# Kernel tuning notes

Hardware: AMD Instinct MI355X
Metric: run time of the kernel (lower is better)

Reference implementation:

```python
import jax, jax.numpy as jnp
import numpy as np

N = 100000
D = 128
E = 1600000
NUM_STEPS = 8
LAM0 = 1.0
LAM1 = 1.0
ALPHA = 1.0 / (1.0 + 0.0 + LAM0 + LAM1)  # args.alp == 0 path


def setup_inputs() -> dict:
    key = jax.random.key(0)
    ks = jax.random.split(key, 12)
    X = jax.random.normal(ks[0], (N, D), dtype=jnp.float32)
    # H init: normal(0, 1/in_features) + I  (notresidual=False branch)
    H1 = jax.random.normal(ks[1], (D, D), dtype=jnp.float32) * (1.0 / D) + jnp.eye(D, dtype=jnp.float32)
    H2 = jax.random.normal(ks[2], (D, D), dtype=jnp.float32) * (1.0 / D) + jnp.eye(D, dtype=jnp.float32)
    w_beta = jax.random.uniform(ks[3], (E,), dtype=jnp.float32)
    w_gamma = jax.random.uniform(ks[4], (E,), dtype=jnp.float32)
    d_beta = jax.random.uniform(ks[5], (N,), dtype=jnp.float32)
    d_gamma = jax.random.uniform(ks[6], (N,), dtype=jnp.float32)
    src_beta = jax.random.randint(ks[7], (E,), 0, N, dtype=jnp.int32)
    dst_beta = jax.random.randint(ks[8], (E,), 0, N, dtype=jnp.int32)
    src_gamma = jax.random.randint(ks[9], (E,), 0, N, dtype=jnp.int32)
    dst_gamma = jax.random.randint(ks[10], (E,), 0, N, dtype=jnp.int32)
    return {"X": X, "H1": H1, "H2": H2, "w_beta": w_beta, "w_gamma": w_gamma,
            "d_beta": d_beta, "d_gamma": d_gamma,
            "src_beta": src_beta, "dst_beta": dst_beta,
            "src_gamma": src_gamma, "dst_gamma": dst_gamma}


def _spmm(w, src, dst, Y):
    # (sparse A) @ Y with A[dst, src] = w
    return jax.ops.segment_sum(w[:, None] * Y[src], dst, num_segments=N)


def reference(X, H1, H2, w_beta, w_gamma, d_beta, d_gamma,
              src_beta, dst_beta, src_gamma, dst_gamma):
    # Q_tild = lam0*D_beta + lam1*D_gamma + I  (diagonal)
    q = LAM0 * d_beta + LAM1 * d_gamma + 1.0  # [N]
    S1 = H1 + H1.T
    P1 = H1 @ H1.T
    S2 = H2 + H2.T
    P2 = H2 @ H2.T
    Y0 = X
    Y = X
    for _ in range(NUM_STEPS):
        AbY = _spmm(w_beta, src_beta, dst_beta, Y)    # A_beta @ Y
        AgY = _spmm(w_gamma, src_gamma, dst_gamma, Y)  # A_gamma @ Y
        term_beta = AbY @ S1 - d_beta[:, None] * (Y @ P1)
        # L_gamma @ Y = D_gamma@Y - A_gamma@Y
        term_gamma = (d_gamma[:, None] * Y - AgY
                      + AgY @ S2 - d_gamma[:, None] * (Y @ P2))
        Y_hat = LAM0 * term_beta + Y0 + LAM1 * term_gamma
        Y = (1.0 - ALPHA) * Y + ALPHA * (Y_hat / q[:, None])
    return Y
```

## Files before the change

### kernel.cpp

```cpp
#include <hip/hip_runtime.h>
#include <cstdint>
#include <cstddef>

#define DD 128
#define ATS 68
#define BQS 132


__global__ void count2_k(const int* __restrict__ dstb, const int* __restrict__ dstg,
                         int* __restrict__ degb, int* __restrict__ degg, int E, int gE) {
    int b = blockIdx.x;
    const int* dst = (b < gE) ? dstb : dstg;
    int* deg = (b < gE) ? degb : degg;
    int i = ((b < gE) ? b : b - gE) * blockDim.x + threadIdx.x;
    if (i < E) atomicAdd(&deg[dst[i]], 1);
}

__global__ __launch_bounds__(1024) void scan2_k(const int* __restrict__ degb,
                                                const int* __restrict__ degg,
                                                int* __restrict__ rpb, int* __restrict__ rpg,
                                                int* __restrict__ curb, int* __restrict__ curg,
                                                int n) {
    const int* deg = (blockIdx.x == 0) ? degb : degg;
    int* rp = (blockIdx.x == 0) ? rpb : rpg;
    int* cur = (blockIdx.x == 0) ? curb : curg;
    __shared__ int sums[1024];
    int tid = threadIdx.x;
    int per = (n + 1023) >> 10;
    int start = tid * per;
    int end = min(start + per, n);
    int s = 0;
    for (int i = start; i < end; ++i) s += deg[i];
    sums[tid] = s;
    __syncthreads();
    for (int off = 1; off < 1024; off <<= 1) {
        int v = (tid >= off) ? sums[tid - off] : 0;
        __syncthreads();
        sums[tid] += v;
        __syncthreads();
    }
    int pre = (tid == 0) ? 0 : sums[tid - 1];
    for (int i = start; i < end; ++i) {
        rp[i] = pre;
        cur[i] = pre;
        pre += deg[i];
    }
    if (end == n) rp[n] = pre;
}

__global__ void fill2_k(const int* __restrict__ srcb, const int* __restrict__ dstb,
                        const float* __restrict__ wb,
                        const int* __restrict__ srcg, const int* __restrict__ dstg,
                        const float* __restrict__ wg,
                        int* __restrict__ curb, int* __restrict__ curg,
                        int2* __restrict__ eb, int2* __restrict__ eg, int E, int gE) {
    int b = blockIdx.x;
    bool isb = (b < gE);
    const int* src = isb ? srcb : srcg;
    const int* dst = isb ? dstb : dstg;
    const float* w = isb ? wb : wg;
    int* cur = isb ? curb : curg;
    int2* edges = isb ? eb : eg;
    int i = (isb ? b : b - gE) * blockDim.x + threadIdx.x;
    if (i < E) {
        int d = dst[i];
        int pos = atomicAdd(&cur[d], 1);
        edges[pos] = make_int2(src[i], __float_as_int(w[i]));
    }
}


__global__ __launch_bounds__(256) void prep_k(const float* __restrict__ H,
                                              float* __restrict__ P,
                                              float* __restrict__ S) {
    int idx = blockIdx.x * 256 + threadIdx.x;
    int i = idx >> 7, j = idx & 127;
    float acc = 0.f;
    for (int k = 0; k < DD; ++k) acc += H[i * DD + k] * H[j * DD + k];
    P[idx] = acc;
    S[idx] = H[i * DD + j] + H[j * DD + i];
}


__global__ __launch_bounds__(256, 8) void spmm2_k(
    const int* __restrict__ rpb, const int2* __restrict__ eb,
    const int* __restrict__ rpg, const int2* __restrict__ eg,
    const float* __restrict__ Y,
    float* __restrict__ outb, float* __restrict__ outg, int n)
{
    int node = blockIdx.x * 4 + (threadIdx.x >> 6);
    if (node >= n) return;
    int lane = threadIdx.x & 63;

    int jb = rpb[node], be = rpb[node + 1];
    int jg = rpg[node], ge = rpg[node + 1];
    float b0 = 0.f, b1 = 0.f, g0 = 0.f, g1 = 0.f;

    while (jb + 4 <= be && jg + 4 <= ge) {
        int2 x0 = eb[jb + 0], x1 = eb[jb + 1], x2 = eb[jb + 2], x3 = eb[jb + 3];
        int2 y0 = eg[jg + 0], y1 = eg[jg + 1], y2 = eg[jg + 2], y3 = eg[jg + 3];
        float2 fb0 = *((const float2*)(Y + (size_t)x0.x * DD) + lane);
        float2 fb1 = *((const float2*)(Y + (size_t)x1.x * DD) + lane);
        float2 fb2 = *((const float2*)(Y + (size_t)x2.x * DD) + lane);
        float2 fb3 = *((const float2*)(Y + (size_t)x3.x * DD) + lane);
        float2 fg0 = *((const float2*)(Y + (size_t)y0.x * DD) + lane);
        float2 fg1 = *((const float2*)(Y + (size_t)y1.x * DD) + lane);
        float2 fg2 = *((const float2*)(Y + (size_t)y2.x * DD) + lane);
        float2 fg3 = *((const float2*)(Y + (size_t)y3.x * DD) + lane);
        float wb0 = __int_as_float(x0.y), wb1 = __int_as_float(x1.y);
        float wb2 = __int_as_float(x2.y), wb3 = __int_as_float(x3.y);
        float wg0 = __int_as_float(y0.y), wg1 = __int_as_float(y1.y);
        float wg2 = __int_as_float(y2.y), wg3 = __int_as_float(y3.y);
        b0 += wb0 * fb0.x; b1 += wb0 * fb0.y;
        b0 += wb1 * fb1.x; b1 += wb1 * fb1.y;
        b0 += wb2 * fb2.x; b1 += wb2 * fb2.y;
        b0 += wb3 * fb3.x; b1 += wb3 * fb3.y;
        g0 += wg0 * fg0.x; g1 += wg0 * fg0.y;
        g0 += wg1 * fg1.x; g1 += wg1 * fg1.y;
        g0 += wg2 * fg2.x; g1 += wg2 * fg2.y;
        g0 += wg3 * fg3.x; g1 += wg3 * fg3.y;
        jb += 4; jg += 4;
    }
    while (jb + 4 <= be) {
        int2 x0 = eb[jb + 0], x1 = eb[jb + 1], x2 = eb[jb + 2], x3 = eb[jb + 3];
        float2 f0 = *((const float2*)(Y + (size_t)x0.x * DD) + lane);
        float2 f1 = *((const float2*)(Y + (size_t)x1.x * DD) + lane);
        float2 f2 = *((const float2*)(Y + (size_t)x2.x * DD) + lane);
        float2 f3 = *((const float2*)(Y + (size_t)x3.x * DD) + lane);
        float w0 = __int_as_float(x0.y), w1 = __int_as_float(x1.y);
        float w2 = __int_as_float(x2.y), w3 = __int_as_float(x3.y);
        b0 += w0 * f0.x; b1 += w0 * f0.y;
        b0 += w1 * f1.x; b1 += w1 * f1.y;
        b0 += w2 * f2.x; b1 += w2 * f2.y;
        b0 += w3 * f3.x; b1 += w3 * f3.y;
        jb += 4;
    }
    while (jg + 4 <= ge) {
        int2 y0 = eg[jg + 0], y1 = eg[jg + 1], y2 = eg[jg + 2], y3 = eg[jg + 3];
        float2 f0 = *((const float2*)(Y + (size_t)y0.x * DD) + lane);
        float2 f1 = *((const float2*)(Y + (size_t)y1.x * DD) + lane);
        float2 f2 = *((const float2*)(Y + (size_t)y2.x * DD) + lane);
        float2 f3 = *((const float2*)(Y + (size_t)y3.x * DD) + lane);
        float w0 = __int_as_float(y0.y), w1 = __int_as_float(y1.y);
        float w2 = __int_as_float(y2.y), w3 = __int_as_float(y3.y);
        g0 += w0 * f0.x; g1 += w0 * f0.y;
        g0 += w1 * f1.x; g1 += w1 * f1.y;
        g0 += w2 * f2.x; g1 += w2 * f2.y;
        g0 += w3 * f3.x; g1 += w3 * f3.y;
        jg += 4;
    }
    for (; jb < be; ++jb) {
        int2 e = eb[jb];
        float2 f = *((const float2*)(Y + (size_t)e.x * DD) + lane);
        float wv = __int_as_float(e.y);
        b0 += wv * f.x; b1 += wv * f.y;
    }
    for (; jg < ge; ++jg) {
        int2 e = eg[jg];
        float2 f = *((const float2*)(Y + (size_t)e.x * DD) + lane);
        float wv = __int_as_float(e.y);
        g0 += wv * f.x; g1 += wv * f.y;
    }
    *((float2*)(outb + (size_t)node * DD) + lane) = make_float2(b0, b1);
    *((float2*)(outg + (size_t)node * DD) + lane) = make_float2(g0, g1);
}


__global__ __launch_bounds__(256, 3) void dense4_k(
    const float* __restrict__ Yc, const float* __restrict__ X,
    const float* __restrict__ AbY, const float* __restrict__ AgY,
    const float* __restrict__ db, const float* __restrict__ dg,
    const float* __restrict__ P1, const float* __restrict__ P2,
    const float* __restrict__ S1, const float* __restrict__ S2,
    float* __restrict__ Yn, int n)
{
    __shared__ float At[DD * ATS];
    __shared__ float U[32 * BQS];

    const int tid = threadIdx.x;
    const int cg = tid & 15;
    const int rg = tid >> 4;
    const int row0 = blockIdx.x * 64;

    float aS[4][8], aP1[4][8], aP2[4][8];
#pragma unroll
    for (int i = 0; i < 4; ++i)
#pragma unroll
        for (int j = 0; j < 8; ++j) { aS[i][j] = 0.f; aP1[i][j] = 0.f; aP2[i][j] = 0.f; }

    auto stageT = [&](const float* __restrict__ G) {
        int r = tid >> 2;
        int rowc = min(row0 + r, n - 1);
        const float* gp = G + (size_t)rowc * DD;
#pragma unroll
        for (int i = 0; i < 8; ++i) {
            int c = ((tid & 3) << 2) + (i << 4);
            float4 v = *reinterpret_cast<const float4*>(gp + c);
            At[(c + 0) * ATS + r] = v.x;
            At[(c + 1) * ATS + r] = v.y;
            At[(c + 2) * ATS + r] = v.z;
            At[(c + 3) * ATS + r] = v.w;
        }
    };
    auto gemm = [&](const float* __restrict__ M, float (&acc)[4][8]) {
#pragma unroll 1
        for (int kq = 0; kq < 4; ++kq) {
            {
                int kl = tid & 31;
                int cb = (tid >> 5) * 16;
                const float* gp = M + (size_t)(kq * 32 + kl) * DD + cb;
                float* bp = U + kl * BQS + cb;
#pragma unroll
                for (int u = 0; u < 4; ++u)
                    *reinterpret_cast<float4*>(bp + 4 * u) =
                        *reinterpret_cast<const float4*>(gp + 4 * u);
            }
            __syncthreads();
#pragma unroll 2
            for (int kl = 0; kl < 32; ++kl) {
                int k = kq * 32 + kl;
                float4 a = *reinterpret_cast<const float4*>(&At[k * ATS + rg * 4]);
                float4 b0 = *reinterpret_cast<const float4*>(&U[kl * BQS + cg * 4]);
                float4 b1 = *reinterpret_cast<const float4*>(&U[kl * BQS + 64 + cg * 4]);
                float av[4] = {a.x, a.y, a.z, a.w};
                float bv[8] = {b0.x, b0.y, b0.z, b0.w, b1.x, b1.y, b1.z, b1.w};
#pragma unroll
                for (int i = 0; i < 4; ++i)
#pragma unroll
                    for (int j = 0; j < 8; ++j) acc[i][j] += av[i] * bv[j];
            }
            __syncthreads();
        }
    };

    stageT(AbY);
    __syncthreads();
    gemm(S1, aS);

    stageT(AgY);
    __syncthreads();
    gemm(S2, aS);
#pragma unroll
    for (int i = 0; i < 4; ++i) {
        int r = rg * 4 + i;
#pragma unroll
        for (int j = 0; j < 8; ++j) {
            int c = (j >> 2) * 64 + cg * 4 + (j & 3);
            aS[i][j] -= At[c * ATS + r];
        }
    }
    __syncthreads();

    stageT(Yc);
    __syncthreads();
    gemm(P1, aP1);
    gemm(P2, aP2);

    const float AL = 1.0f / 3.0f;
#pragma unroll
    for (int i = 0; i < 4; ++i) {
        int row = row0 + rg * 4 + i;
        if (row < n) {
            float dbv = db[row], dgv = dg[row];
            float aq = AL / (dbv + dgv + 1.0f);
#pragma unroll
            for (int hh = 0; hh < 2; ++hh) {
                size_t off = (size_t)row * DD + hh * 64 + cg * 4;
                float4 y = *reinterpret_cast<const float4*>(Yc + off);
                float4 x = *reinterpret_cast<const float4*>(X + off);
                float yv[4] = {y.x, y.y, y.z, y.w};
                float xv[4] = {x.x, x.y, x.z, x.w};
                float ov[4];
#pragma unroll
                for (int q = 0; q < 4; ++q) {
                    int j = hh * 4 + q;
                    float yhat = aS[i][j] + xv[q] + dgv * yv[q]
                                 - dbv * aP1[i][j] - dgv * aP2[i][j];
                    ov[q] = (1.0f - AL) * yv[q] + yhat * aq;
                }
                *reinterpret_cast<float4*>(Yn + off) = make_float4(ov[0], ov[1], ov[2], ov[3]);
            }
        }
    }
}


extern "C" void kernel_launch(void* const* d_in, const int* in_sizes, int n_in,
                              void* d_out, int out_size, void* d_ws, size_t ws_size,
                              hipStream_t stream) {
    const float* X   = (const float*)d_in[0];
    const float* H1  = (const float*)d_in[1];
    const float* H2  = (const float*)d_in[2];
    const float* wb  = (const float*)d_in[3];
    const float* wg  = (const float*)d_in[4];
    const float* db  = (const float*)d_in[5];
    const float* dg  = (const float*)d_in[6];
    const int* srcb  = (const int*)d_in[7];
    const int* dstb  = (const int*)d_in[8];
    const int* srcg  = (const int*)d_in[9];
    const int* dstg  = (const int*)d_in[10];
    const int N = in_sizes[5];
    const int E = in_sizes[3];
    float* Yout = (float*)d_out;

    char* p = (char*)d_ws;
    auto alloc = [&](size_t b) -> void* {
        void* r = (void*)p;
        p += (b + 255) & ~(size_t)255;
        return r;
    };
    float* P1 = (float*)alloc((size_t)DD * DD * 4);
    float* S1 = (float*)alloc((size_t)DD * DD * 4);
    float* P2 = (float*)alloc((size_t)DD * DD * 4);
    float* S2 = (float*)alloc((size_t)DD * DD * 4);
    int* degb = (int*)alloc((size_t)N * 4);
    int* degg = (int*)alloc((size_t)N * 4);
    int* rpb  = (int*)alloc((size_t)(N + 1) * 4);
    int* rpg  = (int*)alloc((size_t)(N + 1) * 4);
    int* curb = (int*)alloc((size_t)N * 4);
    int* curg = (int*)alloc((size_t)N * 4);
    int2* eb  = (int2*)alloc((size_t)E * 8);
    int2* eg  = (int2*)alloc((size_t)E * 8);
    float* AbY = (float*)alloc((size_t)N * DD * 4);
    float* AgY = (float*)alloc((size_t)N * DD * 4);
    float* Yw  = (float*)alloc((size_t)N * DD * 4);

    hipMemsetAsync(degb, 0, (size_t)N * 4, stream);
    hipMemsetAsync(degg, 0, (size_t)N * 4, stream);

    int gE = (E + 255) / 256;
    count2_k<<<2 * gE, 256, 0, stream>>>(dstb, dstg, degb, degg, E, gE);
    scan2_k<<<2, 1024, 0, stream>>>(degb, degg, rpb, rpg, curb, curg, N);
    fill2_k<<<2 * gE, 256, 0, stream>>>(srcb, dstb, wb, srcg, dstg, wg,
                                        curb, curg, eb, eg, E, gE);
    prep_k<<<64, 256, 0, stream>>>(H1, P1, S1);
    prep_k<<<64, 256, 0, stream>>>(H2, P2, S2);

    const float* Ycur = X;
    float* Ybufs[2] = {Yw, Yout};
    int gs = (N + 3) / 4;
    int gd = (N + 63) / 64;
    for (int s = 0; s < 8; ++s) {
        float* Yn = Ybufs[s & 1];
        spmm2_k<<<gs, 256, 0, stream>>>(rpb, eb, rpg, eg, Ycur, AbY, AgY, N);
        dense4_k<<<gd, 256, 0, stream>>>(Ycur, X, AbY, AgY, db, dg,
                                         P1, P2, S1, S2, Yn, N);
        Ycur = Yn;
    }
}
```

Before: 3.955 ms.

## Reorder dense kernel: fused P1/P2 GEMM first, fold into accumulator, prefetch B tiles

The dense update kernel now runs the Y@P1 and Y@P2 GEMMs first in one fused loop over k that shares the A-tile read, then folds them with X, d_gamma*Y and the diagonal terms into a single accumulator. That same accumulator then takes the AbY@S1 and AgY@S2 products, so one 32-float accumulator array is dropped. This lowers register pressure, which matters under launch_bounds(256,3). Both GEMM loops also prefetch the next B tile from global memory into registers while computing on the current one, to hide load latency. In exchange, the fused P loop stages two B tiles per phase and adds more barriers.

```diff
diff --git a/kernel.cpp b/kernel.cpp
--- a/kernel.cpp
+++ b/kernel.cpp
@@ -182,12 +182,6 @@
     const int rg = tid >> 4;
     const int row0 = blockIdx.x * 64;
 
-    float aS[4][8], aP1[4][8], aP2[4][8];
-#pragma unroll
-    for (int i = 0; i < 4; ++i)
-#pragma unroll
-        for (int j = 0; j < 8; ++j) { aS[i][j] = 0.f; aP1[i][j] = 0.f; aP2[i][j] = 0.f; }
-
     auto stageT = [&](const float* __restrict__ G) {
         int r = tid >> 2;
         int rowc = min(row0 + r, n - 1);
@@ -202,26 +196,124 @@
             At[(c + 3) * ATS + r] = v.w;
         }
     };
-    auto gemm = [&](const float* __restrict__ M, float (&acc)[4][8]) {
+
+    float aP1[4][8], aP2[4][8];
+#pragma unroll
+    for (int i = 0; i < 4; ++i)
+#pragma unroll
+        for (int j = 0; j < 8; ++j) { aP1[i][j] = 0.f; aP2[i][j] = 0.f; }
+
+    stageT(Yc);
+
+    {
+        const int kl = tid >> 4;
+        const int cb = (tid & 15) * 8;
+        float4 p1a, p1b, p2a, p2b;
+        {
+            const float* g1 = P1 + (size_t)kl * DD + cb;
+            const float* g2 = P2 + (size_t)kl * DD + cb;
+            p1a = *reinterpret_cast<const float4*>(g1);
+            p1b = *reinterpret_cast<const float4*>(g1 + 4);
+            p2a = *reinterpret_cast<const float4*>(g2);
+            p2b = *reinterpret_cast<const float4*>(g2 + 4);
+        }
+#pragma unroll 1
+        for (int ph = 0; ph < 8; ++ph) {
+            __syncthreads();
+            {
+                float* b1 = U + kl * BQS + cb;
+                float* b2 = U + (16 + kl) * BQS + cb;
+                *reinterpret_cast<float4*>(b1) = p1a;
+                *reinterpret_cast<float4*>(b1 + 4) = p1b;
+                *reinterpret_cast<float4*>(b2) = p2a;
+                *reinterpret_cast<float4*>(b2 + 4) = p2b;
+            }
+            __syncthreads();
+            if (ph < 7) {
+                const float* g1 = P1 + (size_t)((ph + 1) * 16 + kl) * DD + cb;
+                const float* g2 = P2 + (size_t)((ph + 1) * 16 + kl) * DD + cb;
+                p1a = *reinterpret_cast<const float4*>(g1);
+                p1b = *reinterpret_cast<const float4*>(g1 + 4);
+                p2a = *reinterpret_cast<const float4*>(g2);
+                p2b = *reinterpret_cast<const float4*>(g2 + 4);
+            }
+#pragma unroll 2
+            for (int k2 = 0; k2 < 16; ++k2) {
+                int k = ph * 16 + k2;
+                float4 a = *reinterpret_cast<const float4*>(&At[k * ATS + rg * 4]);
+                float4 b10 = *reinterpret_cast<const float4*>(&U[k2 * BQS + cg * 4]);
+                float4 b11 = *reinterpret_cast<const float4*>(&U[k2 * BQS + 64 + cg * 4]);
+                float4 b20 = *reinterpret_cast<const float4*>(&U[(16 + k2) * BQS + cg * 4]);
+                float4 b21 = *reinterpret_cast<const float4*>(&U[(16 + k2) * BQS + 64 + cg * 4]);
+                float av[4] = {a.x, a.y, a.z, a.w};
+                float b1v[8] = {b10.x, b10.y, b10.z, b10.w, b11.x, b11.y, b11.z, b11.w};
+                float b2v[8] = {b20.x, b20.y, b20.z, b20.w, b21.x, b21.y, b21.z, b21.w};
+#pragma unroll
+                for (int i = 0; i < 4; ++i)
+#pragma unroll
+                    for (int j = 0; j < 8; ++j) {
+                        aP1[i][j] += av[i] * b1v[j];
+                        aP2[i][j] += av[i] * b2v[j];
+                    }
+            }
+        }
+        __syncthreads();
+    }
+
+#pragma unroll
+    for (int i = 0; i < 4; ++i) {
+        int rowc = min(row0 + rg * 4 + i, n - 1);
+        float dbv = db[rowc], dgv = dg[rowc];
+#pragma unroll
+        for (int hh = 0; hh < 2; ++hh) {
+            size_t off = (size_t)rowc * DD + hh * 64 + cg * 4;
+            float4 y = *reinterpret_cast<const float4*>(Yc + off);
+            float4 x = *reinterpret_cast<const float4*>(X + off);
+            float yv[4] = {y.x, y.y, y.z, y.w};
+            float xv[4] = {x.x, x.y, x.z, x.w};
+#pragma unroll
+            for (int q = 0; q < 4; ++q) {
+                int j = hh * 4 + q;
+                aP1[i][j] = xv[q] + dgv * yv[q] - dbv * aP1[i][j] - dgv * aP2[i][j];
+            }
+        }
+    }
+
+    auto gemm1 = [&](const float* __restrict__ M, float (&acc)[4][8]) {
+        const int kl = tid & 31;
+        const int cb = (tid >> 5) * 16;
+        float4 pa, pb, pc, pd;
+        {
+            const float* gp = M + (size_t)kl * DD + cb;
+            pa = *reinterpret_cast<const float4*>(gp);
+            pb = *reinterpret_cast<const float4*>(gp + 4);
+            pc = *reinterpret_cast<const float4*>(gp + 8);
+            pd = *reinterpret_cast<const float4*>(gp + 12);
+        }
 #pragma unroll 1
         for (int kq = 0; kq < 4; ++kq) {
+            __syncthreads();
             {
-                int kl = tid & 31;
-                int cb = (tid >> 5) * 16;
-                const float* gp = M + (size_t)(kq * 32 + kl) * DD + cb;
                 float* bp = U + kl * BQS + cb;
-#pragma unroll
-                for (int u = 0; u < 4; ++u)
-                    *reinterpret_cast<float4*>(bp + 4 * u) =
-                        *reinterpret_cast<const float4*>(gp + 4 * u);
+                *reinterpret_cast<float4*>(bp) = pa;
+                *reinterpret_cast<float4*>(bp + 4) = pb;
+                *reinterpret_cast<float4*>(bp + 8) = pc;
+                *reinterpret_cast<float4*>(bp + 12) = pd;
             }
             __syncthreads();
+            if (kq < 3) {
+                const float* gp = M + (size_t)((kq + 1) * 32 + kl) * DD + cb;
+                pa = *reinterpret_cast<const float4*>(gp);
+                pb = *reinterpret_cast<const float4*>(gp + 4);
+                pc = *reinterpret_cast<const float4*>(gp + 8);
+                pd = *reinterpret_cast<const float4*>(gp + 12);
+            }
 #pragma unroll 2
-            for (int kl = 0; kl < 32; ++kl) {
-                int k = kq * 32 + kl;
+            for (int k2 = 0; k2 < 32; ++k2) {
+                int k = kq * 32 + k2;
                 float4 a = *reinterpret_cast<const float4*>(&At[k * ATS + rg * 4]);
-                float4 b0 = *reinterpret_cast<const float4*>(&U[kl * BQS + cg * 4]);
-                float4 b1 = *reinterpret_cast<const float4*>(&U[kl * BQS + 64 + cg * 4]);
+                float4 b0 = *reinterpret_cast<const float4*>(&U[k2 * BQS + cg * 4]);
+                float4 b1 = *reinterpret_cast<const float4*>(&U[k2 * BQS + 64 + cg * 4]);
                 float av[4] = {a.x, a.y, a.z, a.w};
                 float bv[8] = {b0.x, b0.y, b0.z, b0.w, b1.x, b1.y, b1.z, b1.w};
 #pragma unroll
@@ -229,32 +321,24 @@
 #pragma unroll
                     for (int j = 0; j < 8; ++j) acc[i][j] += av[i] * bv[j];
             }
-            __syncthreads();
-        }
+        }
+        __syncthreads();
     };
 
     stageT(AbY);
-    __syncthreads();
-    gemm(S1, aS);
+    gemm1(S1, aP1);
 
     stageT(AgY);
-    __syncthreads();
-    gemm(S2, aS);
+    gemm1(S2, aP1);
 #pragma unroll
     for (int i = 0; i < 4; ++i) {
         int r = rg * 4 + i;
 #pragma unroll
         for (int j = 0; j < 8; ++j) {
             int c = (j >> 2) * 64 + cg * 4 + (j & 3);
-            aS[i][j] -= At[c * ATS + r];
-        }
-    }
-    __syncthreads();
-
-    stageT(Yc);
-    __syncthreads();
-    gemm(P1, aP1);
-    gemm(P2, aP2);
+            aP1[i][j] -= At[c * ATS + r];
+        }
+    }
 
     const float AL = 1.0f / 3.0f;
 #pragma unroll
@@ -267,16 +351,12 @@
             for (int hh = 0; hh < 2; ++hh) {
                 size_t off = (size_t)row * DD + hh * 64 + cg * 4;
                 float4 y = *reinterpret_cast<const float4*>(Yc + off);
-                float4 x = *reinterpret_cast<const float4*>(X + off);
                 float yv[4] = {y.x, y.y, y.z, y.w};
-                float xv[4] = {x.x, x.y, x.z, x.w};
                 float ov[4];
 #pragma unroll
                 for (int q = 0; q < 4; ++q) {
                     int j = hh * 4 + q;
-                    float yhat = aS[i][j] + xv[q] + dgv * yv[q]
-                                 - dbv * aP1[i][j] - dgv * aP2[i][j];
-                    ov[q] = (1.0f - AL) * yv[q] + yhat * aq;
+                    ov[q] = (1.0f - AL) * yv[q] + aP1[i][j] * aq;
                 }
                 *reinterpret_cast<float4*>(Yn + off) = make_float4(ov[0], ov[1], ov[2], ov[3]);
             }
```

Result: no change. 3.916 ms (-1.0%).

## Restructure dense step with wave-uniform weight columns read via scalar loads

Applied to the files above, without the earlier changes.

The dense kernel now runs 1024-thread blocks, one row per lane and 8 output columns per wave. Weight matrix entries are wave-uniform (readfirstlane on the column offset), so they can be fetched with scalar loads instead of being staged through a shared-memory tile, and the P1/P2 products are fused into one pass over the Y tile. Output is transposed through LDS for coalesced stores. The trade-off is a much smaller per-thread register tile (8 accumulators instead of 96), which lowers FMA reuse per LDS read, plus dependence on scalar-cache bandwidth for the weights.

```diff
diff --git a/kernel.cpp b/kernel.cpp
--- a/kernel.cpp
+++ b/kernel.cpp
@@ -4,7 +4,7 @@
 
 #define DD 128
 #define ATS 68
-#define BQS 132
+#define WTS 130
 
 
 __global__ void count2_k(const int* __restrict__ dstb, const int* __restrict__ dstg,
@@ -166,7 +166,7 @@
 }
 
 
-__global__ __launch_bounds__(256, 3) void dense4_k(
+__global__ __launch_bounds__(1024, 8) void dense_vs_k(
     const float* __restrict__ Yc, const float* __restrict__ X,
     const float* __restrict__ AbY, const float* __restrict__ AgY,
     const float* __restrict__ db, const float* __restrict__ dg,
@@ -175,111 +175,121 @@
     float* __restrict__ Yn, int n)
 {
     __shared__ float At[DD * ATS];
-    __shared__ float U[32 * BQS];
-
-    const int tid = threadIdx.x;
-    const int cg = tid & 15;
-    const int rg = tid >> 4;
+
+    const int tid  = threadIdx.x;
+    const int lane = tid & 63;
+    const int wid  = tid >> 6;
+    const int cw   = wid << 3;
+    const int c0   = __builtin_amdgcn_readfirstlane(cw);
     const int row0 = blockIdx.x * 64;
-
-    float aS[4][8], aP1[4][8], aP2[4][8];
-#pragma unroll
-    for (int i = 0; i < 4; ++i)
-#pragma unroll
-        for (int j = 0; j < 8; ++j) { aS[i][j] = 0.f; aP1[i][j] = 0.f; aP2[i][j] = 0.f; }
+    const int rowc = min(row0 + lane, n - 1);
 
     auto stageT = [&](const float* __restrict__ G) {
-        int r = tid >> 2;
-        int rowc = min(row0 + r, n - 1);
-        const float* gp = G + (size_t)rowc * DD;
-#pragma unroll
-        for (int i = 0; i < 8; ++i) {
-            int c = ((tid & 3) << 2) + (i << 4);
-            float4 v = *reinterpret_cast<const float4*>(gp + c);
-            At[(c + 0) * ATS + r] = v.x;
-            At[(c + 1) * ATS + r] = v.y;
-            At[(c + 2) * ATS + r] = v.z;
-            At[(c + 3) * ATS + r] = v.w;
+        const float* gp = G + (size_t)rowc * DD + cw;
+        float4 v0 = *reinterpret_cast<const float4*>(gp);
+        float4 v1 = *reinterpret_cast<const float4*>(gp + 4);
+        At[(cw + 0) * ATS + lane] = v0.x;
+        At[(cw + 1) * ATS + lane] = v0.y;
+        At[(cw + 2) * ATS + lane] = v0.z;
+        At[(cw + 3) * ATS + lane] = v0.w;
+        At[(cw + 4) * ATS + lane] = v1.x;
+        At[(cw + 5) * ATS + lane] = v1.y;
+        At[(cw + 6) * ATS + lane] = v1.z;
+        At[(cw + 7) * ATS + lane] = v1.w;
+    };
+
+    const float dbv = db[rowc];
+    const float dgv = dg[rowc];
+
+    float acc[8];
+
+    stageT(Yc);
+    __syncthreads();
+
+    {
+        const float* xp = X + (size_t)rowc * DD + c0;
+#pragma unroll
+        for (int j = 0; j < 8; ++j)
+            acc[j] = xp[j] + dgv * At[(c0 + j) * ATS + lane];
+    }
+
+    {
+        const float* p1 = P1 + c0;
+        const float* p2 = P2 + c0;
+#pragma unroll 4
+        for (int k = 0; k < DD; ++k) {
+            float a = At[k * ATS + lane];
+            float am1 = dbv * a;
+            float am2 = dgv * a;
+            const float* r1 = p1 + k * DD;
+            const float* r2 = p2 + k * DD;
+#pragma unroll
+            for (int j = 0; j < 8; ++j)
+                acc[j] -= am1 * r1[j] + am2 * r2[j];
         }
-    };
-    auto gemm = [&](const float* __restrict__ M, float (&acc)[4][8]) {
-#pragma unroll 1
-        for (int kq = 0; kq < 4; ++kq) {
-            {
-                int kl = tid & 31;
-                int cb = (tid >> 5) * 16;
-                const float* gp = M + (size_t)(kq * 32 + kl) * DD + cb;
-                float* bp = U + kl * BQS + cb;
-#pragma unroll
-                for (int u = 0; u < 4; ++u)
-                    *reinterpret_cast<float4*>(bp + 4 * u) =
-                        *reinterpret_cast<const float4*>(gp + 4 * u);
-            }
-            __syncthreads();
-#pragma unroll 2
-            for (int kl = 0; kl < 32; ++kl) {
-                int k = kq * 32 + kl;
-                float4 a = *reinterpret_cast<const float4*>(&At[k * ATS + rg * 4]);
-                float4 b0 = *reinterpret_cast<const float4*>(&U[kl * BQS + cg * 4]);
-                float4 b1 = *reinterpret_cast<const float4*>(&U[kl * BQS + 64 + cg * 4]);
-                float av[4] = {a.x, a.y, a.z, a.w};
-                float bv[8] = {b0.x, b0.y, b0.z, b0.w, b1.x, b1.y, b1.z, b1.w};
-#pragma unroll
-                for (int i = 0; i < 4; ++i)
-#pragma unroll
-                    for (int j = 0; j < 8; ++j) acc[i][j] += av[i] * bv[j];
-            }
-            __syncthreads();
+    }
+
+    __syncthreads();
+    stageT(AbY);
+    __syncthreads();
+    {
+        const float* s1 = S1 + c0;
+#pragma unroll 4
+        for (int k = 0; k < DD; ++k) {
+            float a = At[k * ATS + lane];
+            const float* r = s1 + k * DD;
+#pragma unroll
+            for (int j = 0; j < 8; ++j)
+                acc[j] += a * r[j];
         }
-    };
-
-    stageT(AbY);
-    __syncthreads();
-    gemm(S1, aS);
-
+    }
+
+    __syncthreads();
     stageT(AgY);
     __syncthreads();
-    gemm(S2, aS);
-#pragma unroll
-    for (int i = 0; i < 4; ++i) {
-        int r = rg * 4 + i;
-#pragma unroll
-        for (int j = 0; j < 8; ++j) {
-            int c = (j >> 2) * 64 + cg * 4 + (j & 3);
-            aS[i][j] -= At[c * ATS + r];
+    {
+        const float* s2 = S2 + c0;
+#pragma unroll 4
+        for (int k = 0; k < DD; ++k) {
+            float a = At[k * ATS + lane];
+            const float* r = s2 + k * DD;
+#pragma unroll
+            for (int j = 0; j < 8; ++j)
+                acc[j] += a * r[j];
         }
-    }
-    __syncthreads();
-
-    stageT(Yc);
-    __syncthreads();
-    gemm(P1, aP1);
-    gemm(P2, aP2);
-
-    const float AL = 1.0f / 3.0f;
-#pragma unroll
-    for (int i = 0; i < 4; ++i) {
-        int row = row0 + rg * 4 + i;
-        if (row < n) {
-            float dbv = db[row], dgv = dg[row];
-            float aq = AL / (dbv + dgv + 1.0f);
-#pragma unroll
-            for (int hh = 0; hh < 2; ++hh) {
-                size_t off = (size_t)row * DD + hh * 64 + cg * 4;
-                float4 y = *reinterpret_cast<const float4*>(Yc + off);
-                float4 x = *reinterpret_cast<const float4*>(X + off);
-                float yv[4] = {y.x, y.y, y.z, y.w};
-                float xv[4] = {x.x, x.y, x.z, x.w};
-                float ov[4];
-#pragma unroll
-                for (int q = 0; q < 4; ++q) {
-                    int j = hh * 4 + q;
-                    float yhat = aS[i][j] + xv[q] + dgv * yv[q]
-                                 - dbv * aP1[i][j] - dgv * aP2[i][j];
-                    ov[q] = (1.0f - AL) * yv[q] + yhat * aq;
-                }
-                *reinterpret_cast<float4*>(Yn + off) = make_float4(ov[0], ov[1], ov[2], ov[3]);
-            }
+#pragma unroll
+        for (int j = 0; j < 8; ++j)
+            acc[j] -= At[(c0 + j) * ATS + lane];
+    }
+
+    {
+        const float aq = (1.0f / 3.0f) / (dbv + dgv + 1.0f);
+        const float* yp = Yc + (size_t)rowc * DD + c0;
+#pragma unroll
+        for (int j = 0; j < 8; ++j)
+            acc[j] = (2.0f / 3.0f) * yp[j] + acc[j] * aq;
+    }
+
+    __syncthreads();
+    {
+        float* W = At;
+#pragma unroll
+        for (int j = 0; j < 8; ++j)
+            W[lane * WTS + cw + j] = acc[j];
+    }
+    __syncthreads();
+    {
+        const float* W = At;
+        int r2 = tid >> 4;
+        int c2 = (tid & 15) << 3;
+        int row2 = row0 + r2;
+        if (row2 < n) {
+            float ov[8];
+#pragma unroll
+            for (int j = 0; j < 8; ++j) ov[j] = W[r2 * WTS + c2 + j];
+            float* op = Yn + (size_t)row2 * DD + c2;
+            *reinterpret_cast<float4*>(op) = make_float4(ov[0], ov[1], ov[2], ov[3]);
+            *reinterpret_cast<float4*>(op + 4) = make_float4(ov[4], ov[5], ov[6], ov[7]);
         }
     }
 }
@@ -343,8 +353,8 @@
     for (int s = 0; s < 8; ++s) {
         float* Yn = Ybufs[s & 1];
         spmm2_k<<<gs, 256, 0, stream>>>(rpb, eb, rpg, eg, Ycur, AbY, AgY, N);
-        dense4_k<<<gd, 256, 0, stream>>>(Ycur, X, AbY, AgY, db, dg,
-                                         P1, P2, S1, S2, Yn, N);
+        dense_vs_k<<<gd, 1024, 0, stream>>>(Ycur, X, AbY, AgY, db, dg,
+                                            P1, P2, S1, S2, Yn, N);
         Ycur = Yn;
     }
 }
```

New measurement: 4.438 ms. 12.2% more time.

## Fuse dense stage into one K=512 GEMM over concatenated operand matrix

Applied to the files above, without the earlier changes.

Concatenates S1, S2-I, -P1, -P2 into a single 512x128 B matrix and streams [AbY | AgY | db*Y | dg*Y] as a K=512 A operand, so one accumulator replaces three and the -AgY term folds into S2. Shared memory for the A tile shrinks to a 32-row slab, and launch bounds rise to 6 blocks per CU to raise occupancy. The reciprocal q factor is precomputed once into a buffer. The cost is more loop iterations, each with its own sync, and per-element scaling while staging the tile.

```diff
diff --git a/kernel.cpp b/kernel.cpp
--- a/kernel.cpp
+++ b/kernel.cpp
@@ -3,8 +3,8 @@
 #include <cstddef>
 
 #define DD 128
-#define ATS 68
-#define BQS 132
+#define ATS2 68
+#define BQS2 132
 
 
 __global__ void count2_k(const int* __restrict__ dstb, const int* __restrict__ dstg,
@@ -71,14 +71,23 @@
 
 
 __global__ __launch_bounds__(256) void prep_k(const float* __restrict__ H,
-                                              float* __restrict__ P,
-                                              float* __restrict__ S) {
+                                              float* __restrict__ Pdst,
+                                              float* __restrict__ Sdst,
+                                              int sub_ident) {
     int idx = blockIdx.x * 256 + threadIdx.x;
     int i = idx >> 7, j = idx & 127;
     float acc = 0.f;
     for (int k = 0; k < DD; ++k) acc += H[i * DD + k] * H[j * DD + k];
-    P[idx] = acc;
-    S[idx] = H[i * DD + j] + H[j * DD + i];
+    Pdst[idx] = -acc;
+    float s = H[i * DD + j] + H[j * DD + i];
+    if (sub_ident && i == j) s -= 1.0f;
+    Sdst[idx] = s;
+}
+
+__global__ void aq_k(const float* __restrict__ db, const float* __restrict__ dg,
+                     float* __restrict__ aq, int n) {
+    int i = blockIdx.x * blockDim.x + threadIdx.x;
+    if (i < n) aq[i] = (1.0f / 3.0f) / (db[i] + dg[i] + 1.0f);
 }
 
 
@@ -166,103 +175,86 @@
 }
 
 
-__global__ __launch_bounds__(256, 3) void dense4_k(
+__global__ __launch_bounds__(256, 6) void denseBig_k(
     const float* __restrict__ Yc, const float* __restrict__ X,
     const float* __restrict__ AbY, const float* __restrict__ AgY,
     const float* __restrict__ db, const float* __restrict__ dg,
-    const float* __restrict__ P1, const float* __restrict__ P2,
-    const float* __restrict__ S1, const float* __restrict__ S2,
+    const float* __restrict__ Bcat, const float* __restrict__ aq,
     float* __restrict__ Yn, int n)
 {
-    __shared__ float At[DD * ATS];
-    __shared__ float U[32 * BQS];
+    __shared__ float At[32 * ATS2];
+    __shared__ float U[32 * BQS2];
 
     const int tid = threadIdx.x;
     const int cg = tid & 15;
     const int rg = tid >> 4;
     const int row0 = blockIdx.x * 64;
 
-    float aS[4][8], aP1[4][8], aP2[4][8];
+    const int sr = tid >> 2;
+    const int sq = (tid & 3) * 8;
+    const int srow = min(row0 + sr, n - 1);
+    const float dbr = db[srow];
+    const float dgr = dg[srow];
+
+    const int bkl = tid & 31;
+    const int bcb = (tid >> 5) * 16;
+
+    float acc[4][8];
 #pragma unroll
     for (int i = 0; i < 4; ++i)
 #pragma unroll
-        for (int j = 0; j < 8; ++j) { aS[i][j] = 0.f; aP1[i][j] = 0.f; aP2[i][j] = 0.f; }
-
-    auto stageT = [&](const float* __restrict__ G) {
-        int r = tid >> 2;
-        int rowc = min(row0 + r, n - 1);
-        const float* gp = G + (size_t)rowc * DD;
-#pragma unroll
-        for (int i = 0; i < 8; ++i) {
-            int c = ((tid & 3) << 2) + (i << 4);
-            float4 v = *reinterpret_cast<const float4*>(gp + c);
-            At[(c + 0) * ATS + r] = v.x;
-            At[(c + 1) * ATS + r] = v.y;
-            At[(c + 2) * ATS + r] = v.z;
-            At[(c + 3) * ATS + r] = v.w;
+        for (int j = 0; j < 8; ++j) acc[i][j] = 0.f;
+
+#pragma unroll 1
+    for (int p = 0; p < 16; ++p) {
+        const int part = p >> 2;
+        const float* src = (part == 0) ? AbY : (part == 1) ? AgY : Yc;
+        const float scale = (part == 0 || part == 1) ? 1.0f : (part == 2 ? dbr : dgr);
+        const int kbase = (p & 3) * 32;
+
+        if (p) __syncthreads();
+        {
+            const float* gp = src + (size_t)srow * DD + kbase + sq;
+            float4 v0 = *reinterpret_cast<const float4*>(gp);
+            float4 v1 = *reinterpret_cast<const float4*>(gp + 4);
+            At[(sq + 0) * ATS2 + sr] = scale * v0.x;
+            At[(sq + 1) * ATS2 + sr] = scale * v0.y;
+            At[(sq + 2) * ATS2 + sr] = scale * v0.z;
+            At[(sq + 3) * ATS2 + sr] = scale * v0.w;
+            At[(sq + 4) * ATS2 + sr] = scale * v1.x;
+            At[(sq + 5) * ATS2 + sr] = scale * v1.y;
+            At[(sq + 6) * ATS2 + sr] = scale * v1.z;
+            At[(sq + 7) * ATS2 + sr] = scale * v1.w;
         }
-    };
-    auto gemm = [&](const float* __restrict__ M, float (&acc)[4][8]) {
-#pragma unroll 1
-        for (int kq = 0; kq < 4; ++kq) {
-            {
-                int kl = tid & 31;
-                int cb = (tid >> 5) * 16;
-                const float* gp = M + (size_t)(kq * 32 + kl) * DD + cb;
-                float* bp = U + kl * BQS + cb;
-#pragma unroll
-                for (int u = 0; u < 4; ++u)
-                    *reinterpret_cast<float4*>(bp + 4 * u) =
-                        *reinterpret_cast<const float4*>(gp + 4 * u);
-            }
-            __syncthreads();
+        {
+            const float* gp = Bcat + (size_t)(p * 32 + bkl) * DD + bcb;
+            float* bp = U + bkl * BQS2 + bcb;
+            *reinterpret_cast<float4*>(bp)      = *reinterpret_cast<const float4*>(gp);
+            *reinterpret_cast<float4*>(bp + 4)  = *reinterpret_cast<const float4*>(gp + 4);
+            *reinterpret_cast<float4*>(bp + 8)  = *reinterpret_cast<const float4*>(gp + 8);
+            *reinterpret_cast<float4*>(bp + 12) = *reinterpret_cast<const float4*>(gp + 12);
+        }
+        __syncthreads();
 #pragma unroll 2
-            for (int kl = 0; kl < 32; ++kl) {
-                int k = kq * 32 + kl;
-                float4 a = *reinterpret_cast<const float4*>(&At[k * ATS + rg * 4]);
-                float4 b0 = *reinterpret_cast<const float4*>(&U[kl * BQS + cg * 4]);
-                float4 b1 = *reinterpret_cast<const float4*>(&U[kl * BQS + 64 + cg * 4]);
-                float av[4] = {a.x, a.y, a.z, a.w};
-                float bv[8] = {b0.x, b0.y, b0.z, b0.w, b1.x, b1.y, b1.z, b1.w};
-#pragma unroll
-                for (int i = 0; i < 4; ++i)
-#pragma unroll
-                    for (int j = 0; j < 8; ++j) acc[i][j] += av[i] * bv[j];
-            }
-            __syncthreads();
+        for (int k2 = 0; k2 < 32; ++k2) {
+            float4 a  = *reinterpret_cast<const float4*>(&At[k2 * ATS2 + rg * 4]);
+            float4 b0 = *reinterpret_cast<const float4*>(&U[k2 * BQS2 + cg * 4]);
+            float4 b1 = *reinterpret_cast<const float4*>(&U[k2 * BQS2 + 64 + cg * 4]);
+            float av[4] = {a.x, a.y, a.z, a.w};
+            float bv[8] = {b0.x, b0.y, b0.z, b0.w, b1.x, b1.y, b1.z, b1.w};
+#pragma unroll
+            for (int i = 0; i < 4; ++i)
+#pragma unroll
+                for (int j = 0; j < 8; ++j) acc[i][j] += av[i] * bv[j];
         }
-    };
-
-    stageT(AbY);
-    __syncthreads();
-    gemm(S1, aS);
-
-    stageT(AgY);
-    __syncthreads();
-    gemm(S2, aS);
-#pragma unroll
-    for (int i = 0; i < 4; ++i) {
-        int r = rg * 4 + i;
-#pragma unroll
-        for (int j = 0; j < 8; ++j) {
-            int c = (j >> 2) * 64 + cg * 4 + (j & 3);
-            aS[i][j] -= At[c * ATS + r];
-        }
-    }
-    __syncthreads();
-
-    stageT(Yc);
-    __syncthreads();
-    gemm(P1, aP1);
-    gemm(P2, aP2);
-
-    const float AL = 1.0f / 3.0f;
+    }
+
 #pragma unroll
     for (int i = 0; i < 4; ++i) {
         int row = row0 + rg * 4 + i;
         if (row < n) {
-            float dbv = db[row], dgv = dg[row];
-            float aq = AL / (dbv + dgv + 1.0f);
+            float aqv = aq[row];
+            float dgv = dg[row];
 #pragma unroll
             for (int hh = 0; hh < 2; ++hh) {
                 size_t off = (size_t)row * DD + hh * 64 + cg * 4;
@@ -274,9 +266,7 @@
 #pragma unroll
                 for (int q = 0; q < 4; ++q) {
                     int j = hh * 4 + q;
-                    float yhat = aS[i][j] + xv[q] + dgv * yv[q]
-                                 - dbv * aP1[i][j] - dgv * aP2[i][j];
-                    ov[q] = (1.0f - AL) * yv[q] + yhat * aq;
+                    ov[q] = (2.0f / 3.0f) * yv[q] + (acc[i][j] + xv[q] + dgv * yv[q]) * aqv;
                 }
                 *reinterpret_cast<float4*>(Yn + off) = make_float4(ov[0], ov[1], ov[2], ov[3]);
             }
@@ -309,16 +299,14 @@
         p += (b + 255) & ~(size_t)255;
         return r;
     };
-    float* P1 = (float*)alloc((size_t)DD * DD * 4);
-    float* S1 = (float*)alloc((size_t)DD * DD * 4);
-    float* P2 = (float*)alloc((size_t)DD * DD * 4);
-    float* S2 = (float*)alloc((size_t)DD * DD * 4);
+    float* Bcat = (float*)alloc((size_t)512 * DD * 4);
     int* degb = (int*)alloc((size_t)N * 4);
     int* degg = (int*)alloc((size_t)N * 4);
     int* rpb  = (int*)alloc((size_t)(N + 1) * 4);
     int* rpg  = (int*)alloc((size_t)(N + 1) * 4);
     int* curb = (int*)alloc((size_t)N * 4);
     int* curg = (int*)alloc((size_t)N * 4);
+    float* aq = (float*)alloc((size_t)N * 4);
     int2* eb  = (int2*)alloc((size_t)E * 8);
     int2* eg  = (int2*)alloc((size_t)E * 8);
     float* AbY = (float*)alloc((size_t)N * DD * 4);
@@ -328,13 +316,19 @@
     hipMemsetAsync(degb, 0, (size_t)N * 4, stream);
     hipMemsetAsync(degg, 0, (size_t)N * 4, stream);
 
+    float* S1s  = Bcat;
+    float* S2s  = Bcat + 128 * DD;
+    float* P1s  = Bcat + 256 * DD;
+    float* P2s  = Bcat + 384 * DD;
+
     int gE = (E + 255) / 256;
     count2_k<<<2 * gE, 256, 0, stream>>>(dstb, dstg, degb, degg, E, gE);
     scan2_k<<<2, 1024, 0, stream>>>(degb, degg, rpb, rpg, curb, curg, N);
     fill2_k<<<2 * gE, 256, 0, stream>>>(srcb, dstb, wb, srcg, dstg, wg,
                                         curb, curg, eb, eg, E, gE);
-    prep_k<<<64, 256, 0, stream>>>(H1, P1, S1);
-    prep_k<<<64, 256, 0, stream>>>(H2, P2, S2);
+    prep_k<<<64, 256, 0, stream>>>(H1, P1s, S1s, 0);
+    prep_k<<<64, 256, 0, stream>>>(H2, P2s, S2s, 1);
+    aq_k<<<(N + 255) / 256, 256, 0, stream>>>(db, dg, aq, N);
 
     const float* Ycur = X;
     float* Ybufs[2] = {Yw, Yout};
@@ -343,8 +337,8 @@
     for (int s = 0; s < 8; ++s) {
         float* Yn = Ybufs[s & 1];
         spmm2_k<<<gs, 256, 0, stream>>>(rpb, eb, rpg, eg, Ycur, AbY, AgY, N);
-        dense4_k<<<gd, 256, 0, stream>>>(Ycur, X, AbY, AgY, db, dg,
-                                         P1, P2, S1, S2, Yn, N);
+        denseBig_k<<<gd, 256, 0, stream>>>(Ycur, X, AbY, AgY, db, dg,
+                                           Bcat, aq, Yn, N);
         Ycur = Yn;
     }
 }
```

After: 3.895 ms. No clear change (-1.5%).
